# Optimization experiments

Hardware: AMD Instinct MI355X
Metric: run time of the kernel (lower is better)

## Reference

```python
import jax, jax.numpy as jnp
import numpy as np

N = 262144      # number of 3D points
D = 128         # in_channels
NCLS = 20       # classes
M = 10          # num_prototype
EPS = 0.05      # sinkhorn epsilon
ITERS = 3       # sinkhorn iterations
GAMMA = 0.99    # EMA momentum
LN_EPS = 1e-5

def layer_norm(x, g, b):
    mu = jnp.mean(x, axis=-1, keepdims=True)
    v = jnp.mean((x - mu) ** 2, axis=-1, keepdims=True)
    return (x - mu) / jnp.sqrt(v + LN_EPS) * g + b

def l2n(x):
    # F.normalize(p=2, dim=-1) with eps=1e-12
    return x / jnp.clip(jnp.linalg.norm(x, axis=-1, keepdims=True), 1e-12)

def setup_inputs() -> dict:
    key = jax.random.key(0)
    k1, k2, k3 = jax.random.split(key, 3)
    return {
        "feature3d": jax.random.normal(k1, (N, D), dtype=jnp.float32),
        "gt_seg": jax.random.randint(k2, (N,), 0, NCLS, dtype=jnp.int32),
        "prototypes": jax.random.normal(k3, (NCLS, M, D), dtype=jnp.float32),
        "feat_gamma": jnp.ones((D,), jnp.float32),
        "feat_beta": jnp.zeros((D,), jnp.float32),
        "mask_gamma": jnp.ones((NCLS,), jnp.float32),
        "mask_beta": jnp.zeros((NCLS,), jnp.float32),
    }

def reference(feature3d, gt_seg, prototypes, feat_gamma, feat_beta, mask_gamma, mask_beta):
    _c = l2n(layer_norm(feature3d, feat_gamma, feat_beta))            # [N,D]
    protos = l2n(prototypes)                                          # [K,M,D]
    masks = jnp.einsum('nd,kmd->nmk', _c, protos)                     # [N,M,K]
    out_seg = layer_norm(jnp.max(masks, axis=1), mask_gamma, mask_beta)  # [N,K]

    # ---- prototype_learning ----
    pred = jnp.argmax(out_seg, axis=-1)
    correct = (gt_seg == pred).astype(_c.dtype)                       # [N]
    proto_logits = _c @ protos.reshape(-1, D).T                       # [N,K*M]

    sel = jax.nn.one_hot(gt_seg, NCLS, dtype=_c.dtype)                # [N,K]
    # masked per-class sinkhorn, vectorized across all 20 classes
    L = jnp.exp(jnp.transpose(masks, (2, 1, 0)) / EPS) * sel.T[:, None, :]  # [K,M,N]
    B = jnp.sum(sel, axis=0)                                          # [K] points per class
    s = jnp.sum(L, axis=(1, 2), keepdims=True)
    L = L / jnp.where(s > 0, s, 1.0)
    Bsafe = jnp.where(B > 0, B, 1.0)[:, None, None]
    for _ in range(ITERS):
        rs = jnp.sum(L, axis=2, keepdims=True)                        # per-prototype row sum
        L = L / (jnp.where(rs > 0, rs, 1.0) * M)
        cs = jnp.sum(L, axis=1, keepdims=True)                        # per-point col sum
        L = L / jnp.where(cs > 0, cs, 1.0) / Bsafe
    L = L * B[:, None, None]

    idx = jnp.argmax(L, axis=1)                                       # [K,N] hard assignment
    q = jax.nn.one_hot(idx, M, dtype=_c.dtype)                        # [K,N,M] (one_hot(argmax))

    w = sel.T * correct[None, :]                                      # [K,N] class-k AND correct
    m_q = q * w[:, :, None]                                           # [K,N,M]
    f = jnp.einsum('knm,nd->kmd', m_q, _c * correct[:, None])         # [K,M,D]
    ncount = jnp.sum(m_q, axis=1)                                     # [K,M]
    fn = l2n(f)
    upd = GAMMA * protos + (1.0 - GAMMA) * fn                         # momentum_update
    new_protos = l2n(jnp.where(ncount[..., None] > 0, upd, protos))   # [K,M,D]

    idx_pp = idx[gt_seg, jnp.arange(N)]                               # per-point proto index
    proto_target = (idx_pp + M * gt_seg).astype(jnp.float32)          # [N]
    return out_seg, proto_logits, proto_target, new_protos
```

## Files before the change

kernel.cpp:

```cpp
#include <hip/hip_runtime.h>
#include <hip/hip_bf16.h>

#define NPTS 262144
#define DIM  128
#define KC   20
#define MP   10
#define LNEPS 1e-5f
#define EPSI  0.05f
#define CCAP  65536

typedef _Float16 half8 __attribute__((ext_vector_type(8)));
typedef float f32x4 __attribute__((ext_vector_type(4)));

union H8U4 { half8 h; uint4 u; };

#define WS_PN     0
#define WS_PHI    25600
#define WS_PLO    39936
#define WS_F      54272
#define WS_NCOUNT 79872
#define WS_CCNT   80072
#define WS_UH     80080
#define WS_SK     80680
#define WS_BC     80700
#define WS_PSB    80720
#define WS_PR     162640
#define WS_EXPV   367440
#define WS_CIDX   3513168

#define MFMA_(b_, a_, c_) __builtin_amdgcn_mfma_f32_16x16x32_f16(b_, a_, c_, 0, 0, 0)

__device__ __forceinline__ half8 lds_h8(const uint4* p) {
    return *reinterpret_cast<const half8*>(p);
}

__device__ __forceinline__ void gload_lds16(const uint4* g, uint4* l) {
    __builtin_amdgcn_global_load_lds(
        (const __attribute__((address_space(1))) void*)(g),
        (__attribute__((address_space(3))) void*)(l), 16, 0, 0);
}

__global__ __launch_bounds__(64) void k_norm_protos(
    const float* __restrict__ pr, float* __restrict__ pn,
    _Float16* __restrict__ phi, _Float16* __restrict__ plo)
{
    int j = blockIdx.x, l = threadIdx.x;
    const int jm = j & 15;
    const int s1 = l >> 3,       swz1 = (((s1 ^ jm) << 3) | (l & 7));
    const int s2 = 8 + (l >> 3), swz2 = (((s2 ^ jm) << 3) | (l & 7));
    if (j < 200) {
        float x0 = pr[(size_t)j*128 + l], x1 = pr[(size_t)j*128 + 64 + l];
        float ss = x0*x0 + x1*x1;
        #pragma unroll
        for (int off = 32; off > 0; off >>= 1) ss += __shfl_xor(ss, off);
        float dn = fmaxf(sqrtf(ss), 1e-12f);
        float y0 = x0/dn, y1 = x1/dn;
        pn[(size_t)j*128 + l]      = y0;
        pn[(size_t)j*128 + 64 + l] = y1;
        _Float16 h0 = (_Float16)y0, h1 = (_Float16)y1;
        phi[(size_t)j*128 + swz1] = h0;
        phi[(size_t)j*128 + swz2] = h1;
        plo[(size_t)j*128 + swz1] = (_Float16)(y0 - (float)h0);
        plo[(size_t)j*128 + swz2] = (_Float16)(y1 - (float)h1);
    } else {
        phi[(size_t)j*128 + swz1] = (_Float16)0.f;  phi[(size_t)j*128 + swz2] = (_Float16)0.f;
        plo[(size_t)j*128 + swz1] = (_Float16)0.f;  plo[(size_t)j*128 + swz2] = (_Float16)0.f;
    }
}

__global__ __launch_bounds__(256, 2) void k_main(
    const float* __restrict__ feat, const int* __restrict__ gt,
    const _Float16* __restrict__ phi, const _Float16* __restrict__ plo,
    const float* __restrict__ fg, const float* __restrict__ fb,
    const float* __restrict__ mg, const float* __restrict__ mb,
    float* __restrict__ out_seg, float* __restrict__ plog,
    float* __restrict__ expv, float* __restrict__ psb,
    int* __restrict__ cidx, int* __restrict__ ccnt)
{
    __shared__ __align__(16) char ldsb[49152];
    __shared__ float sumS[128];
    __shared__ int   gtS[128];
    __shared__ float part[320];
    uint4* bbuf = (uint4*)ldsb;
    float* epi  = (float*)ldsb;

    const int t = threadIdx.x, blk = blockIdx.x;
    const int w = t >> 6, lane = t & 63;
    const int l15 = lane & 15, l4 = lane >> 4;
    const int pbase = blk * 128;

    const uint4* phi4 = (const uint4*)phi;
    const uint4* plo4 = (const uint4*)plo;

#define STAGE_B(S, BI) do { \
        const uint4* gh = phi4 + (size_t)(S)*512 + (w*64 + lane); \
        const uint4* gl = plo4 + (size_t)(S)*512 + (w*64 + lane); \
        uint4* dh = bbuf + (BI)*1024 + w*64; \
        uint4* dl = bbuf + (BI)*1024 + 512 + w*64; \
        gload_lds16(gh,       dh); \
        gload_lds16(gh + 256, dh + 256); \
        gload_lds16(gl,       dl); \
        gload_lds16(gl + 256, dl + 256); \
    } while (0)

    STAGE_B(0, 0);
    STAGE_B(1, 1);

    const float4* gfeat = (const float4*)feat;
    float4 A[2][4][2];
    #pragma unroll
    for (int mt = 0; mt < 2; ++mt) {
        size_t rb = (size_t)(pbase + w*32 + mt*16 + l15) * 32;
        #pragma unroll
        for (int kst = 0; kst < 4; ++kst)
            #pragma unroll
            for (int h = 0; h < 2; ++h)
                A[mt][kst][h] = gfeat[rb + kst*8 + l4*2 + h];
    }
    float4 G[4][2], Bb[4][2];
    {
        const float4* fg4 = (const float4*)fg;
        const float4* fb4 = (const float4*)fb;
        #pragma unroll
        for (int kst = 0; kst < 4; ++kst)
            #pragma unroll
            for (int h = 0; h < 2; ++h) {
                G[kst][h]  = fg4[kst*8 + l4*2 + h];
                Bb[kst][h] = fb4[kst*8 + l4*2 + h];
            }
    }

    half8 fah[2][4], fal[2][4];
    #pragma unroll
    for (int mt = 0; mt < 2; ++mt) {
        float s0 = 0.f;
        #pragma unroll
        for (int kst = 0; kst < 4; ++kst)
            #pragma unroll
            for (int h = 0; h < 2; ++h) {
                float4 v = A[mt][kst][h];
                s0 += v.x + v.y + v.z + v.w;
            }
        s0 += __shfl_xor(s0, 16); s0 += __shfl_xor(s0, 32);
        float mean = s0 * (1.f/128.f);
        float s1 = 0.f;
        #pragma unroll
        for (int kst = 0; kst < 4; ++kst)
            #pragma unroll
            for (int h = 0; h < 2; ++h) {
                float4 v = A[mt][kst][h];
                float a = v.x-mean, b = v.y-mean, c = v.z-mean, d = v.w-mean;
                s1 += a*a + b*b + c*c + d*d;
            }
        s1 += __shfl_xor(s1, 16); s1 += __shfl_xor(s1, 32);
        float rstd = rsqrtf(s1 * (1.f/128.f) + LNEPS);
        float s2 = 0.f;
        #pragma unroll
        for (int kst = 0; kst < 4; ++kst)
            #pragma unroll
            for (int h = 0; h < 2; ++h) {
                float4 v = A[mt][kst][h];
                float4 g = G[kst][h], bb = Bb[kst][h];
                v.x = (v.x-mean)*rstd*g.x + bb.x;
                v.y = (v.y-mean)*rstd*g.y + bb.y;
                v.z = (v.z-mean)*rstd*g.z + bb.z;
                v.w = (v.w-mean)*rstd*g.w + bb.w;
                A[mt][kst][h] = v;
                s2 += v.x*v.x + v.y*v.y + v.z*v.z + v.w*v.w;
            }
        s2 += __shfl_xor(s2, 16); s2 += __shfl_xor(s2, 32);
        float rl2 = 1.f / fmaxf(sqrtf(s2), 1e-12f);
        #pragma unroll
        for (int kst = 0; kst < 4; ++kst) {
            float4 va = A[mt][kst][0], vb = A[mt][kst][1];
            va.x*=rl2; va.y*=rl2; va.z*=rl2; va.w*=rl2;
            vb.x*=rl2; vb.y*=rl2; vb.z*=rl2; vb.w*=rl2;
            H8U4 h, lo;
            h.h[0]=(_Float16)va.x; h.h[1]=(_Float16)va.y; h.h[2]=(_Float16)va.z; h.h[3]=(_Float16)va.w;
            h.h[4]=(_Float16)vb.x; h.h[5]=(_Float16)vb.y; h.h[6]=(_Float16)vb.z; h.h[7]=(_Float16)vb.w;
            lo.h[0]=(_Float16)(va.x-(float)h.h[0]); lo.h[1]=(_Float16)(va.y-(float)h.h[1]);
            lo.h[2]=(_Float16)(va.z-(float)h.h[2]); lo.h[3]=(_Float16)(va.w-(float)h.h[3]);
            lo.h[4]=(_Float16)(vb.x-(float)h.h[4]); lo.h[5]=(_Float16)(vb.y-(float)h.h[5]);
            lo.h[6]=(_Float16)(vb.z-(float)h.h[6]); lo.h[7]=(_Float16)(vb.w-(float)h.h[7]);
            fah[mt][kst] = h.h;
            fal[mt][kst] = lo.h;
        }
    }

    f32x4 acc[2][13];
    #pragma unroll
    for (int mt = 0; mt < 2; ++mt)
        #pragma unroll
        for (int nt = 0; nt < 13; ++nt)
            acc[mt][nt] = (f32x4){0.f,0.f,0.f,0.f};

    __syncthreads();

    #pragma unroll
    for (int s = 0; s < 7; ++s) {
        if (s < 5) STAGE_B(s + 2, (s + 2) % 3);
        const uint4* bb = bbuf + (s % 3)*1024;
        if (s < 6) {
            #pragma unroll
            for (int kst = 0; kst < 4; ++kst) {
                const int slz = (kst*4 + l4) ^ l15;
                half8 b0h = lds_h8(bb + l15*16 + slz);
                half8 b0l = lds_h8(bb + 512 + l15*16 + slz);
                half8 b1h = lds_h8(bb + (16+l15)*16 + slz);
                half8 b1l = lds_h8(bb + 512 + (16+l15)*16 + slz);
                acc[0][2*s]   = MFMA_(b0h, fah[0][kst], acc[0][2*s]);
                acc[1][2*s]   = MFMA_(b0h, fah[1][kst], acc[1][2*s]);
                acc[0][2*s+1] = MFMA_(b1h, fah[0][kst], acc[0][2*s+1]);
                acc[1][2*s+1] = MFMA_(b1h, fah[1][kst], acc[1][2*s+1]);
                acc[0][2*s]   = MFMA_(b0h, fal[0][kst], acc[0][2*s]);
                acc[1][2*s]   = MFMA_(b0h, fal[1][kst], acc[1][2*s]);
                acc[0][2*s+1] = MFMA_(b1h, fal[0][kst], acc[0][2*s+1]);
                acc[1][2*s+1] = MFMA_(b1h, fal[1][kst], acc[1][2*s+1]);
                acc[0][2*s]   = MFMA_(b0l, fah[0][kst], acc[0][2*s]);
                acc[1][2*s]   = MFMA_(b0l, fah[1][kst], acc[1][2*s]);
                acc[0][2*s+1] = MFMA_(b1l, fah[0][kst], acc[0][2*s+1]);
                acc[1][2*s+1] = MFMA_(b1l, fah[1][kst], acc[1][2*s+1]);
                acc[0][2*s]   = MFMA_(b0l, fal[0][kst], acc[0][2*s]);
                acc[1][2*s]   = MFMA_(b0l, fal[1][kst], acc[1][2*s]);
                acc[0][2*s+1] = MFMA_(b1l, fal[0][kst], acc[0][2*s+1]);
                acc[1][2*s+1] = MFMA_(b1l, fal[1][kst], acc[1][2*s+1]);
            }
        } else {
            #pragma unroll
            for (int kst = 0; kst < 4; ++kst) {
                const int slz = (kst*4 + l4) ^ l15;
                half8 b0h = lds_h8(bb + l15*16 + slz);
                half8 b0l = lds_h8(bb + 512 + l15*16 + slz);
                acc[0][12] = MFMA_(b0h, fah[0][kst], acc[0][12]);
                acc[1][12] = MFMA_(b0h, fah[1][kst], acc[1][12]);
                acc[0][12] = MFMA_(b0h, fal[0][kst], acc[0][12]);
                acc[1][12] = MFMA_(b0h, fal[1][kst], acc[1][12]);
                acc[0][12] = MFMA_(b0l, fah[0][kst], acc[0][12]);
                acc[1][12] = MFMA_(b0l, fah[1][kst], acc[1][12]);
                acc[0][12] = MFMA_(b0l, fal[0][kst], acc[0][12]);
                acc[1][12] = MFMA_(b0l, fal[1][kst], acc[1][12]);
            }
        }
        __syncthreads();
    }

    #pragma unroll 1
    for (int p = 0; p < 4; ++p) {
        if (w == p) {
            #pragma unroll
            for (int mt = 0; mt < 2; ++mt)
                #pragma unroll
                for (int nt = 0; nt < 13; ++nt)
                    if (nt < 12 || l4 < 2) {
                        float4 sv;
                        sv.x = acc[mt][nt][0]; sv.y = acc[mt][nt][1];
                        sv.z = acc[mt][nt][2]; sv.w = acc[mt][nt][3];
                        *reinterpret_cast<float4*>(
                            &epi[(mt*16 + l15)*210 + nt*16 + l4*4]) = sv;
                    }
        }
        __syncthreads();
        if (t < 128) {
            const int q = t >> 2, sub = t & 3;
            const int n = pbase + p*32 + q;
            float ml[5];
            #pragma unroll
            for (int kk = 0; kk < 5; ++kk) {
                int k = sub*5 + kk;
                float mx = epi[q*210 + k*10];
                #pragma unroll
                for (int m = 1; m < 10; ++m) mx = fmaxf(mx, epi[q*210 + k*10 + m]);
                ml[kk] = mx;
            }
            float s0 = ml[0]+ml[1]+ml[2]+ml[3]+ml[4];
            s0 += __shfl_xor(s0,1); s0 += __shfl_xor(s0,2);
            float mean = s0 / 20.f;
            float s1 = 0.f;
            #pragma unroll
            for (int kk = 0; kk < 5; ++kk) { float d = ml[kk]-mean; s1 += d*d; }
            s1 += __shfl_xor(s1,1); s1 += __shfl_xor(s1,2);
            float rstd = rsqrtf(s1 / 20.f + LNEPS);
            float bv = -1e30f; int bk = 0;
            #pragma unroll
            for (int kk = 0; kk < 5; ++kk) {
                int k = sub*5 + kk;
                float y = (ml[kk]-mean)*rstd*mg[k] + mb[k];
                out_seg[(size_t)n*20 + k] = y;
                if (y > bv) { bv = y; bk = k; }
            }
            #pragma unroll
            for (int off = 1; off <= 2; off <<= 1) {
                float ov = __shfl_xor(bv, off);
                int   ok = __shfl_xor(bk, off);
                if (ov > bv || (ov == bv && ok < bk)) { bv = ov; bk = ok; }
            }
            int g = gt[n];
            if (sub == 0) {
                if (bk == g) {
                    int slot = atomicAdd(ccnt, 1);
                    if (slot < CCAP) cidx[slot] = n;
                }
                float se = 0.f;
                #pragma unroll
                for (int m = 0; m < 10; ++m) {
                    float e = expf(epi[q*210 + g*10 + m] / EPSI);
                    expv[(size_t)n*12 + m] = e;
                    se += e;
                }
                sumS[p*32 + q] = se;
                gtS[p*32 + q]  = g;
            }
        }
        __syncthreads();
    }

    if (t < 160) {
        int c = t >> 3, o = t & 7;
        float cnt = 0.f, sm = 0.f;
        for (int i = o*16; i < o*16 + 16; ++i)
            if (gtS[i] == c) { cnt += 1.f; sm += sumS[i]; }
        part[t] = cnt; part[160 + t] = sm;
    }
    __syncthreads();
    if (t < 20) {
        float cnt = 0.f, sm = 0.f;
        #pragma unroll
        for (int o = 0; o < 8; ++o) { cnt += part[t*8+o]; sm += part[160 + t*8+o]; }
        psb[(size_t)t*2048 + blk]      = cnt;
        psb[(size_t)(20+t)*2048 + blk] = sm;
    }

    #pragma unroll
    for (int mt = 0; mt < 2; ++mt)
        #pragma unroll
        for (int nt = 0; nt < 13; ++nt)
            if (nt < 12 || l4 < 2) {
                float4 sv;
                sv.x = acc[mt][nt][0]; sv.y = acc[mt][nt][1];
                sv.z = acc[mt][nt][2]; sv.w = acc[mt][nt][3];
                *reinterpret_cast<float4*>(
                    &plog[(size_t)(pbase + w*32 + mt*16 + l15)*200 + nt*16 + l4*4]) = sv;
            }
#undef STAGE_B
}

__global__ __launch_bounds__(256) void k_reduce_sB(
    const float* __restrict__ psb, float* __restrict__ sk, float* __restrict__ Bc)
{
    __shared__ float red[256];
    int t = threadIdx.x, rrow = blockIdx.x;
    float s = 0.f;
    #pragma unroll
    for (int i = 0; i < 8; ++i) s += psb[(size_t)rrow*2048 + i*256 + t];
    red[t] = s; __syncthreads();
    for (int off = 128; off > 0; off >>= 1) { if (t < off) red[t] += red[t+off]; __syncthreads(); }
    if (t == 0) { if (rrow < 20) Bc[rrow] = red[0]; else sk[rrow-20] = red[0]; }
}

__global__ __launch_bounds__(256) void k_row(int iter,
    const int* __restrict__ gt, const float* __restrict__ expv,
    const float* __restrict__ uh, const float* __restrict__ sk,
    const float* __restrict__ Bc, float* __restrict__ pr)
{
    __shared__ float prodS[2560];
    __shared__ int gtS[256];
    int t = threadIdx.x, b = blockIdx.x;
    int n = b*256 + t;
    int g = gt[n];
    float e[10];
    {
        const float4* e4 = (const float4*)(expv + (size_t)n*12);
        float4 ea = e4[0], eb = e4[1], ec = e4[2];
        e[0]=ea.x; e[1]=ea.y; e[2]=ea.z; e[3]=ea.w;
        e[4]=eb.x; e[5]=eb.y; e[6]=eb.z; e[7]=eb.w;
        e[8]=ec.x; e[9]=ec.y;
    }
    float skg = sk[g];
    float v = (skg > 0.f) ? 1.f/skg : 1.f;
    float B = Bc[g];
    float Bs = (B > 0.f) ? B : 1.f;
    for (int c = 1; c < iter; ++c) {
        const float* uc = uh + (c-1)*200 + g*10;
        float sc = 0.f;
        #pragma unroll
        for (int m = 0; m < 10; ++m) sc += e[m]*uc[m];
        v = (sc > 0.f) ? 1.f/(Bs*sc) : v/Bs;
    }
    #pragma unroll
    for (int m = 0; m < 10; ++m) prodS[t*10+m] = e[m]*v;
    gtS[t] = g;
    __syncthreads();
    if (t < 200) {
        int kk = t / 10, mm = t % 10;
        float acc = 0.f;
        for (int i = 0; i < 256; ++i)
            if (gtS[i] == kk) acc += prodS[i*10+mm];
        pr[(size_t)t*1024 + b] = acc;
    }
}

__global__ __launch_bounds__(256) void k_reduce_u(int iter,
    const float* __restrict__ pr, float* __restrict__ uh)
{
    __shared__ float red[256];
    int t = threadIdx.x, j = blockIdx.x;
    float s = 0.f;
    #pragma unroll
    for (int i = 0; i < 4; ++i) s += pr[(size_t)j*1024 + i*256 + t];
    red[t] = s; __syncthreads();
    for (int off = 128; off > 0; off >>= 1) { if (t < off) red[t] += red[t+off]; __syncthreads(); }
    if (t == 0) {
        float S = red[0];
        float uprev = (iter == 1) ? 1.f : uh[(iter-2)*200 + j];
        uh[(iter-1)*200 + j] = (S > 0.f) ? 1.f/(10.f*S) : uprev*0.1f;
    }
}

__global__ __launch_bounds__(256) void k_post(
    const int* __restrict__ gt, const float* __restrict__ expv,
    const float* __restrict__ u,
    const int* __restrict__ cidx, const int* __restrict__ ccnt,
    const float* __restrict__ feat, const float* __restrict__ fg,
    const float* __restrict__ fb,
    float* __restrict__ ptarget, float* __restrict__ facc,
    float* __restrict__ ncount)
{
    int t = threadIdx.x;
    {
        int n = blockIdx.x*256 + t;
        int g = gt[n];
        const float* uk = u + g*10;
        float bv = -1e30f; int idx = 0;
        #pragma unroll
        for (int m = 0; m < 10; ++m) {
            float pm = expv[(size_t)n*12 + m] * uk[m];
            if (pm > bv) { bv = pm; idx = m; }
        }
        ptarget[n] = (float)(idx + 10*g);
    }
    int wid = blockIdx.x*4 + (t >> 6);
    int lane = t & 63;
    int cnt = *ccnt; if (cnt > CCAP) cnt = CCAP;
    for (int i = wid; i < cnt; i += 4096) {
        int n = cidx[i];
        float x0 = feat[(size_t)n*128 + lane], x1 = feat[(size_t)n*128 + 64 + lane];
        float s = x0 + x1;
        #pragma unroll
        for (int off = 32; off > 0; off >>= 1) s += __shfl_xor(s, off);
        float mean = s * (1.f/128.f);
        float d0 = x0 - mean, d1 = x1 - mean;
        float s2 = d0*d0 + d1*d1;
        #pragma unroll
        for (int off = 32; off > 0; off >>= 1) s2 += __shfl_xor(s2, off);
        float rstd = rsqrtf(s2 * (1.f/128.f) + LNEPS);
        float y0 = d0*rstd*fg[lane] + fb[lane];
        float y1 = d1*rstd*fg[64+lane] + fb[64+lane];
        float s3 = y0*y0 + y1*y1;
        #pragma unroll
        for (int off = 32; off > 0; off >>= 1) s3 += __shfl_xor(s3, off);
        float rl2 = 1.f / fmaxf(sqrtf(s3), 1e-12f);
        float c0 = y0*rl2, c1 = y1*rl2;
        int g = gt[n];
        const float* uk = u + g*10;
        float bv = -1e30f; int idx = 0;
        #pragma unroll
        for (int m = 0; m < 10; ++m) {
            float pm = expv[(size_t)n*12 + m] * uk[m];
            if (pm > bv) { bv = pm; idx = m; }
        }
        float* frow = facc + (size_t)(g*10+idx)*128;
        atomicAdd(&frow[lane], c0);
        atomicAdd(&frow[64+lane], c1);
        if (lane == 0) atomicAdd(&ncount[g*10+idx], 1.f);
    }
}

__global__ __launch_bounds__(64) void k_proto_update(
    const float* __restrict__ facc, const float* __restrict__ ncount,
    const float* __restrict__ pn, float* __restrict__ outp)
{
    const float OMG = (float)(1.0 - 0.99);
    int j = blockIdx.x, l = threadIdx.x;
    float f0 = facc[(size_t)j*128+l], f1 = facc[(size_t)j*128+64+l];
    float ss = f0*f0 + f1*f1;
    #pragma unroll
    for (int off = 32; off > 0; off >>= 1) ss += __shfl_xor(ss, off);
    float fl2 = fmaxf(sqrtf(ss), 1e-12f);
    float fn0 = f0/fl2, fn1 = f1/fl2;
    float p0 = pn[(size_t)j*128+l], p1 = pn[(size_t)j*128+64+l];
    float u0 = 0.99f*p0 + OMG*fn0, u1 = 0.99f*p1 + OMG*fn1;
    bool ok = ncount[j] > 0.f;
    float s0 = ok ? u0 : p0, s1 = ok ? u1 : p1;
    float ss2 = s0*s0 + s1*s1;
    #pragma unroll
    for (int off = 32; off > 0; off >>= 1) ss2 += __shfl_xor(ss2, off);
    float l2 = fmaxf(sqrtf(ss2), 1e-12f);
    outp[(size_t)j*128+l]      = s0/l2;
    outp[(size_t)j*128+64+l]   = s1/l2;
}

extern "C" void kernel_launch(void* const* d_in, const int* in_sizes, int n_in,
                              void* d_out, int out_size, void* d_ws, size_t ws_size,
                              hipStream_t stream)
{
    const float* feat   = (const float*)d_in[0];
    const int*   gt     = (const int*)  d_in[1];
    const float* protos = (const float*)d_in[2];
    const float* fg     = (const float*)d_in[3];
    const float* fb     = (const float*)d_in[4];
    const float* mg     = (const float*)d_in[5];
    const float* mb     = (const float*)d_in[6];

    float* out      = (float*)d_out;
    float* out_seg  = out;
    float* plog     = out + (size_t)NPTS*20;
    float* ptarget  = out + (size_t)NPTS*220;
    float* newp     = out + (size_t)NPTS*221;

    float* ws   = (float*)d_ws;
    float* pn   = ws + WS_PN;
    _Float16* phi = (_Float16*)(ws + WS_PHI);
    _Float16* plo = (_Float16*)(ws + WS_PLO);
    float* facc = ws + WS_F;
    float* ncnt = ws + WS_NCOUNT;
    int*   ccnt = (int*)(ws + WS_CCNT);
    float* uh   = ws + WS_UH;
    float* sk   = ws + WS_SK;
    float* Bc   = ws + WS_BC;
    float* psb  = ws + WS_PSB;
    float* pr   = ws + WS_PR;
    float* expv = ws + WS_EXPV;
    int*   cidx = (int*)(ws + WS_CIDX);

    hipMemsetAsync(facc, 0, (25600 + 200 + 8)*sizeof(float), stream);
    hipLaunchKernelGGL(k_norm_protos, dim3(224), dim3(64), 0, stream, protos, pn, phi, plo);
    hipLaunchKernelGGL(k_main, dim3(2048), dim3(256), 0, stream,
                       feat, gt, phi, plo, fg, fb, mg, mb, out_seg, plog, expv, psb,
                       cidx, ccnt);
    hipLaunchKernelGGL(k_reduce_sB, dim3(40), dim3(256), 0, stream, psb, sk, Bc);
    for (int it = 1; it <= 3; ++it) {
        hipLaunchKernelGGL(k_row, dim3(1024), dim3(256), 0, stream, it, gt, expv, uh, sk, Bc, pr);
        hipLaunchKernelGGL(k_reduce_u, dim3(200), dim3(256), 0, stream, it, pr, uh);
    }
    hipLaunchKernelGGL(k_post, dim3(1024), dim3(256), 0, stream,
                       gt, expv, uh + 400, cidx, ccnt, feat, fg, fb, ptarget, facc, ncnt);
    hipLaunchKernelGGL(k_proto_update, dim3(200), dim3(64), 0, stream, facc, ncnt, pn, newp);
}
```

Baseline: 273.4 us.

## Halve points per block in k_main to cut registers and raise occupancy

```diff
diff --git a/kernel.cpp b/kernel.cpp
--- a/kernel.cpp
+++ b/kernel.cpp
@@ -24,9 +24,9 @@
 #define WS_SK     80680
 #define WS_BC     80700
 #define WS_PSB    80720
-#define WS_PR     162640
-#define WS_EXPV   367440
-#define WS_CIDX   3513168
+#define WS_PR     244560
+#define WS_EXPV   449360
+#define WS_CIDX   3595088
 
 #define MFMA_(b_, a_, c_) __builtin_amdgcn_mfma_f32_16x16x32_f16(b_, a_, c_, 0, 0, 0)
 
@@ -68,7 +68,7 @@
     }
 }
 
-__global__ __launch_bounds__(256, 2) void k_main(
+__global__ __launch_bounds__(256, 3) void k_main(
     const float* __restrict__ feat, const int* __restrict__ gt,
     const _Float16* __restrict__ phi, const _Float16* __restrict__ plo,
     const float* __restrict__ fg, const float* __restrict__ fb,
@@ -78,8 +78,8 @@
     int* __restrict__ cidx, int* __restrict__ ccnt)
 {
     __shared__ __align__(16) char ldsb[49152];
-    __shared__ float sumS[128];
-    __shared__ int   gtS[128];
+    __shared__ float sumS[64];
+    __shared__ int   gtS[64];
     __shared__ float part[320];
     uint4* bbuf = (uint4*)ldsb;
     float* epi  = (float*)ldsb;
@@ -87,14 +87,14 @@
     const int t = threadIdx.x, blk = blockIdx.x;
     const int w = t >> 6, lane = t & 63;
     const int l15 = lane & 15, l4 = lane >> 4;
-    const int pbase = blk * 128;
+    const int pbase = blk * 64;
 
     const uint4* phi4 = (const uint4*)phi;
     const uint4* plo4 = (const uint4*)plo;
 
 #define STAGE_B(S, BI) do { \
-        const uint4* gh = phi4 + (size_t)(S)*512 + (w*64 + lane); \
-        const uint4* gl = plo4 + (size_t)(S)*512 + (w*64 + lane); \
+        const uint4* gh = phi4 + (size_t)(S)*512 + t; \
+        const uint4* gl = plo4 + (size_t)(S)*512 + t; \
         uint4* dh = bbuf + (BI)*1024 + w*64; \
         uint4* dl = bbuf + (BI)*1024 + 512 + w*64; \
         gload_lds16(gh,       dh); \
@@ -107,15 +107,14 @@
     STAGE_B(1, 1);
 
     const float4* gfeat = (const float4*)feat;
-    float4 A[2][4][2];
-    #pragma unroll
-    for (int mt = 0; mt < 2; ++mt) {
-        size_t rb = (size_t)(pbase + w*32 + mt*16 + l15) * 32;
+    float4 A[4][2];
+    {
+        size_t rb = (size_t)(pbase + w*16 + l15) * 32;
         #pragma unroll
         for (int kst = 0; kst < 4; ++kst)
             #pragma unroll
             for (int h = 0; h < 2; ++h)
-                A[mt][kst][h] = gfeat[rb + kst*8 + l4*2 + h];
+                A[kst][h] = gfeat[rb + kst*8 + l4*2 + h];
     }
     float4 G[4][2], Bb[4][2];
     {
@@ -130,15 +129,14 @@
             }
     }
 
-    half8 fah[2][4], fal[2][4];
-    #pragma unroll
-    for (int mt = 0; mt < 2; ++mt) {
+    half8 fah[4], fal[4];
+    {
         float s0 = 0.f;
         #pragma unroll
         for (int kst = 0; kst < 4; ++kst)
             #pragma unroll
             for (int h = 0; h < 2; ++h) {
-                float4 v = A[mt][kst][h];
+                float4 v = A[kst][h];
                 s0 += v.x + v.y + v.z + v.w;
             }
         s0 += __shfl_xor(s0, 16); s0 += __shfl_xor(s0, 32);
@@ -148,7 +146,7 @@
         for (int kst = 0; kst < 4; ++kst)
             #pragma unroll
             for (int h = 0; h < 2; ++h) {
-                float4 v = A[mt][kst][h];
+                float4 v = A[kst][h];
                 float a = v.x-mean, b = v.y-mean, c = v.z-mean, d = v.w-mean;
                 s1 += a*a + b*b + c*c + d*d;
             }
@@ -159,20 +157,20 @@
         for (int kst = 0; kst < 4; ++kst)
             #pragma unroll
             for (int h = 0; h < 2; ++h) {
-                float4 v = A[mt][kst][h];
+                float4 v = A[kst][h];
                 float4 g = G[kst][h], bb = Bb[kst][h];
                 v.x = (v.x-mean)*rstd*g.x + bb.x;
                 v.y = (v.y-mean)*rstd*g.y + bb.y;
                 v.z = (v.z-mean)*rstd*g.z + bb.z;
                 v.w = (v.w-mean)*rstd*g.w + bb.w;
-                A[mt][kst][h] = v;
+                A[kst][h] = v;
                 s2 += v.x*v.x + v.y*v.y + v.z*v.z + v.w*v.w;
             }
         s2 += __shfl_xor(s2, 16); s2 += __shfl_xor(s2, 32);
         float rl2 = 1.f / fmaxf(sqrtf(s2), 1e-12f);
         #pragma unroll
         for (int kst = 0; kst < 4; ++kst) {
-            float4 va = A[mt][kst][0], vb = A[mt][kst][1];
+            float4 va = A[kst][0], vb = A[kst][1];
             va.x*=rl2; va.y*=rl2; va.z*=rl2; va.w*=rl2;
             vb.x*=rl2; vb.y*=rl2; vb.z*=rl2; vb.w*=rl2;
             H8U4 h, lo;
@@ -182,17 +180,15 @@
             lo.h[2]=(_Float16)(va.z-(float)h.h[2]); lo.h[3]=(_Float16)(va.w-(float)h.h[3]);
             lo.h[4]=(_Float16)(vb.x-(float)h.h[4]); lo.h[5]=(_Float16)(vb.y-(float)h.h[5]);
             lo.h[6]=(_Float16)(vb.z-(float)h.h[6]); lo.h[7]=(_Float16)(vb.w-(float)h.h[7]);
-            fah[mt][kst] = h.h;
-            fal[mt][kst] = lo.h;
-        }
-    }
-
-    f32x4 acc[2][13];
-    #pragma unroll
-    for (int mt = 0; mt < 2; ++mt)
-        #pragma unroll
-        for (int nt = 0; nt < 13; ++nt)
-            acc[mt][nt] = (f32x4){0.f,0.f,0.f,0.f};
+            fah[kst] = h.h;
+            fal[kst] = lo.h;
+        }
+    }
+
+    f32x4 acc[13];
+    #pragma unroll
+    for (int nt = 0; nt < 13; ++nt)
+        acc[nt] = (f32x4){0.f,0.f,0.f,0.f};
 
     __syncthreads();
 
@@ -208,22 +204,14 @@
                 half8 b0l = lds_h8(bb + 512 + l15*16 + slz);
                 half8 b1h = lds_h8(bb + (16+l15)*16 + slz);
                 half8 b1l = lds_h8(bb + 512 + (16+l15)*16 + slz);
-                acc[0][2*s]   = MFMA_(b0h, fah[0][kst], acc[0][2*s]);
-                acc[1][2*s]   = MFMA_(b0h, fah[1][kst], acc[1][2*s]);
-                acc[0][2*s+1] = MFMA_(b1h, fah[0][kst], acc[0][2*s+1]);
-                acc[1][2*s+1] = MFMA_(b1h, fah[1][kst], acc[1][2*s+1]);
-                acc[0][2*s]   = MFMA_(b0h, fal[0][kst], acc[0][2*s]);
-                acc[1][2*s]   = MFMA_(b0h, fal[1][kst], acc[1][2*s]);
-                acc[0][2*s+1] = MFMA_(b1h, fal[0][kst], acc[0][2*s+1]);
-                acc[1][2*s+1] = MFMA_(b1h, fal[1][kst], acc[1][2*s+1]);
-                acc[0][2*s]   = MFMA_(b0l, fah[0][kst], acc[0][2*s]);
-                acc[1][2*s]   = MFMA_(b0l, fah[1][kst], acc[1][2*s]);
-                acc[0][2*s+1] = MFMA_(b1l, fah[0][kst], acc[0][2*s+1]);
-                acc[1][2*s+1] = MFMA_(b1l, fah[1][kst], acc[1][2*s+1]);
-                acc[0][2*s]   = MFMA_(b0l, fal[0][kst], acc[0][2*s]);
-                acc[1][2*s]   = MFMA_(b0l, fal[1][kst], acc[1][2*s]);
-                acc[0][2*s+1] = MFMA_(b1l, fal[0][kst], acc[0][2*s+1]);
-                acc[1][2*s+1] = MFMA_(b1l, fal[1][kst], acc[1][2*s+1]);
+                acc[2*s]   = MFMA_(b0h, fah[kst], acc[2*s]);
+                acc[2*s+1] = MFMA_(b1h, fah[kst], acc[2*s+1]);
+                acc[2*s]   = MFMA_(b0h, fal[kst], acc[2*s]);
+                acc[2*s+1] = MFMA_(b1h, fal[kst], acc[2*s+1]);
+                acc[2*s]   = MFMA_(b0l, fah[kst], acc[2*s]);
+                acc[2*s+1] = MFMA_(b1l, fah[kst], acc[2*s+1]);
+                acc[2*s]   = MFMA_(b0l, fal[kst], acc[2*s]);
+                acc[2*s+1] = MFMA_(b1l, fal[kst], acc[2*s+1]);
             }
         } else {
             #pragma unroll
@@ -231,33 +219,27 @@
                 const int slz = (kst*4 + l4) ^ l15;
                 half8 b0h = lds_h8(bb + l15*16 + slz);
                 half8 b0l = lds_h8(bb + 512 + l15*16 + slz);
-                acc[0][12] = MFMA_(b0h, fah[0][kst], acc[0][12]);
-                acc[1][12] = MFMA_(b0h, fah[1][kst], acc[1][12]);
-                acc[0][12] = MFMA_(b0h, fal[0][kst], acc[0][12]);
-                acc[1][12] = MFMA_(b0h, fal[1][kst], acc[1][12]);
-                acc[0][12] = MFMA_(b0l, fah[0][kst], acc[0][12]);
-                acc[1][12] = MFMA_(b0l, fah[1][kst], acc[1][12]);
-                acc[0][12] = MFMA_(b0l, fal[0][kst], acc[0][12]);
-                acc[1][12] = MFMA_(b0l, fal[1][kst], acc[1][12]);
+                acc[12] = MFMA_(b0h, fah[kst], acc[12]);
+                acc[12] = MFMA_(b0h, fal[kst], acc[12]);
+                acc[12] = MFMA_(b0l, fah[kst], acc[12]);
+                acc[12] = MFMA_(b0l, fal[kst], acc[12]);
             }
         }
         __syncthreads();
     }
 
     #pragma unroll 1
-    for (int p = 0; p < 4; ++p) {
-        if (w == p) {
-            #pragma unroll
-            for (int mt = 0; mt < 2; ++mt)
-                #pragma unroll
-                for (int nt = 0; nt < 13; ++nt)
-                    if (nt < 12 || l4 < 2) {
-                        float4 sv;
-                        sv.x = acc[mt][nt][0]; sv.y = acc[mt][nt][1];
-                        sv.z = acc[mt][nt][2]; sv.w = acc[mt][nt][3];
-                        *reinterpret_cast<float4*>(
-                            &epi[(mt*16 + l15)*210 + nt*16 + l4*4]) = sv;
-                    }
+    for (int p = 0; p < 2; ++p) {
+        if ((w >> 1) == p) {
+            int row = (w & 1)*16 + l15;
+            #pragma unroll
+            for (int nt = 0; nt < 13; ++nt)
+                if (nt < 12 || l4 < 2) {
+                    float4 sv;
+                    sv.x = acc[nt][0]; sv.y = acc[nt][1];
+                    sv.z = acc[nt][2]; sv.w = acc[nt][3];
+                    *reinterpret_cast<float4*>(&epi[row*210 + nt*16 + l4*4]) = sv;
+                }
         }
         __syncthreads();
         if (t < 128) {
@@ -317,7 +299,7 @@
     if (t < 160) {
         int c = t >> 3, o = t & 7;
         float cnt = 0.f, sm = 0.f;
-        for (int i = o*16; i < o*16 + 16; ++i)
+        for (int i = o*8; i < o*8 + 8; ++i)
             if (gtS[i] == c) { cnt += 1.f; sm += sumS[i]; }
         part[t] = cnt; part[160 + t] = sm;
     }
@@ -326,21 +308,19 @@
         float cnt = 0.f, sm = 0.f;
         #pragma unroll
         for (int o = 0; o < 8; ++o) { cnt += part[t*8+o]; sm += part[160 + t*8+o]; }
-        psb[(size_t)t*2048 + blk]      = cnt;
-        psb[(size_t)(20+t)*2048 + blk] = sm;
-    }
-
-    #pragma unroll
-    for (int mt = 0; mt < 2; ++mt)
-        #pragma unroll
-        for (int nt = 0; nt < 13; ++nt)
-            if (nt < 12 || l4 < 2) {
-                float4 sv;
-                sv.x = acc[mt][nt][0]; sv.y = acc[mt][nt][1];
-                sv.z = acc[mt][nt][2]; sv.w = acc[mt][nt][3];
-                *reinterpret_cast<float4*>(
-                    &plog[(size_t)(pbase + w*32 + mt*16 + l15)*200 + nt*16 + l4*4]) = sv;
-            }
+        psb[(size_t)t*4096 + blk]      = cnt;
+        psb[(size_t)(20+t)*4096 + blk] = sm;
+    }
+
+    #pragma unroll
+    for (int nt = 0; nt < 13; ++nt)
+        if (nt < 12 || l4 < 2) {
+            float4 sv;
+            sv.x = acc[nt][0]; sv.y = acc[nt][1];
+            sv.z = acc[nt][2]; sv.w = acc[nt][3];
+            *reinterpret_cast<float4*>(
+                &plog[(size_t)(pbase + w*16 + l15)*200 + nt*16 + l4*4]) = sv;
+        }
 #undef STAGE_B
 }
 
@@ -351,7 +331,7 @@
     int t = threadIdx.x, rrow = blockIdx.x;
     float s = 0.f;
     #pragma unroll
-    for (int i = 0; i < 8; ++i) s += psb[(size_t)rrow*2048 + i*256 + t];
+    for (int i = 0; i < 16; ++i) s += psb[(size_t)rrow*4096 + i*256 + t];
     red[t] = s; __syncthreads();
     for (int off = 128; off > 0; off >>= 1) { if (t < off) red[t] += red[t+off]; __syncthreads(); }
     if (t == 0) { if (rrow < 20) Bc[rrow] = red[0]; else sk[rrow-20] = red[0]; }
@@ -534,7 +514,7 @@
 
     hipMemsetAsync(facc, 0, (25600 + 200 + 8)*sizeof(float), stream);
     hipLaunchKernelGGL(k_norm_protos, dim3(224), dim3(64), 0, stream, protos, pn, phi, plo);
-    hipLaunchKernelGGL(k_main, dim3(2048), dim3(256), 0, stream,
+    hipLaunchKernelGGL(k_main, dim3(4096), dim3(256), 0, stream,
                        feat, gt, phi, plo, fg, fb, mg, mb, out_seg, plog, expv, psb,
                        cidx, ccnt);
     hipLaunchKernelGGL(k_reduce_sB, dim3(40), dim3(256), 0, stream, psb, sk, Bc);
```

Result: no change. 270.2 us (-1.2%).
